# Kernel optimization log

Measured on AMD Instinct MI355X. Metric: run time of the kernel, lower is better.

Reference implementation:

```python
import jax, jax.numpy as jnp
import numpy as np

B = 2048
U_DIM = 128
N_USER = 500000
N_NEWS = 50000
N_WORD = 279215
TITLE_LEN = 10
W_EMB = 50
U_NB = 30   # user_neighbor
N_NB = 30   # news_neighbor
NCAPS = 8
NHID = 16
DIM = NCAPS * NHID          # 128
CNN_OUT = 128
ROUTIT = 4
CONV_CH, KH, KW = 8, 2, 20
PH, PW = 2, 1
FLAT = CONV_CH * ((TITLE_LEN - KH + 1) // PH) * (W_EMB - KW + 1)  # 8*4*31 = 992


def setup_inputs() -> dict:
    key = jax.random.key(0)
    ks = jax.random.split(key, 18)
    nrm = lambda k, s: jax.random.normal(k, s, jnp.float32) * 0.1
    return {
        "user_indices": jax.random.randint(ks[0], (B,), 0, N_USER),
        "news_indices": jax.random.randint(ks[1], (B,), 0, N_NEWS),
        "labels": (jax.random.uniform(ks[2], (B,)) > 0.5).astype(jnp.float32),
        # int neighbor / title tables (module buffers)
        "news_user": jax.random.randint(ks[3], (N_NEWS + 1, U_NB), 0, N_USER),
        "user_news": jax.random.randint(ks[4], (N_USER + 1, N_NB), 0, N_NEWS),
        "title": jax.random.randint(ks[5], (N_NEWS + 1, TITLE_LEN), 0, N_WORD),
        # float parameters
        "user_emb_matrix": nrm(ks[6], (N_USER + 1, U_DIM)),
        "word_emb_matrix": nrm(ks[7], (N_WORD + 1, W_EMB)),
        "conv_w": nrm(ks[8], (CONV_CH, 1, KH, KW)),
        "conv_b": jnp.zeros((CONV_CH,), jnp.float32),
        "dense_w": nrm(ks[9], (FLAT, CNN_OUT)),
        "dense_b": jnp.zeros((CNN_OUT,), jnp.float32),
        "user_weights": nrm(ks[10], (U_DIM, DIM)),
        "user_bias": nrm(ks[11], (DIM,)),
        "item_weights": nrm(ks[12], (CNN_OUT, DIM)),
        "item_bias": nrm(ks[13], (DIM,)),
        "last_w": nrm(ks[14], (DIM, DIM)),
        "last_b": jnp.zeros((DIM,), jnp.float32),
    }


def _convolution(news_ids, title, word_emb, conv_w, conv_b, dense_w, dense_b):
    """Title-CNN news encoder. news_ids: [B, K] int -> [B*K, CNN_OUT]."""
    bk = news_ids.shape[0] * news_ids.shape[1]
    words = title[news_ids.reshape(-1)]              # [BK, L] gather
    x = word_emb[words][:, None, :, :]               # [BK, 1, L, 50]
    y = jax.lax.conv_general_dilated(
        x, conv_w, (1, 1), 'VALID', dimension_numbers=('NCHW', 'OIHW', 'NCHW'))
    y = jax.nn.relu(y + conv_b[None, :, None, None])
    y = jax.lax.reduce_window(y, -jnp.inf, jax.lax.max,
                              (1, 1, PH, PW), (1, 1, PH, PW), 'VALID')
    return jax.nn.relu(y.reshape(bk, -1) @ dense_w + dense_b)


def _routing(x_self, z_nb):
    """Capsule neighbor routing. x_self: [B, DIM], z_nb: [B, K, DIM]."""
    l2n = lambda v: v / (jnp.linalg.norm(v, axis=-1, keepdims=True) + 1e-9)
    x = l2n(x_self.reshape(-1, NCAPS, NHID))
    z = l2n(z_nb.reshape(z_nb.shape[0], z_nb.shape[1], NCAPS, NHID))
    u = x
    for _ in range(ROUTIT):
        p = jax.nn.softmax(jnp.einsum('bkcd,bcd->bkc', z, u), axis=-1)  # over caps
        u = l2n(x + jnp.einsum('bkc,bkcd->bcd', p, z))
    return u.reshape(-1, DIM)


def reference(user_indices, news_indices, labels, news_user, user_news, title,
              user_emb_matrix, word_emb_matrix, conv_w, conv_b, dense_w, dense_b,
              user_weights, user_bias, item_weights, item_bias, last_w, last_b):
    # hop-0 (seed) vectors
    news_v0 = jax.nn.relu(
        _convolution(news_indices[:, None], title, word_emb_matrix,
                     conv_w, conv_b, dense_w, dense_b) @ item_weights + item_bias)  # [B, DIM]
    user_v0 = jax.nn.relu(user_emb_matrix[user_indices] @ user_weights + user_bias)  # [B, DIM]
    # hop-1 neighbor gathers
    news_nb = news_user[news_indices]   # [B, U_NB] user ids clicked this news
    user_nb = user_news[user_indices]   # [B, N_NB] news ids clicked by user
    news_v1 = jax.nn.relu(user_emb_matrix[news_nb] @ user_weights + user_bias)  # [B, U_NB, DIM]
    user_v1 = jax.nn.relu(
        _convolution(user_nb, title, word_emb_matrix, conv_w, conv_b,
                     dense_w, dense_b) @ item_weights + item_bias
    ).reshape(B, N_NB, DIM)
    # capsule routing aggregation
    news_emb = _routing(news_v0, news_v1)
    user_emb = _routing(user_v0, user_v1)
    # simple_dot_net scoring
    x_map = user_emb @ last_w + last_b
    y_map = news_emb @ last_w + last_b
    scores = jnp.sum(x_map * y_map, axis=-1)
    return jax.nn.sigmoid(scores)
```

## Files before the change

### kernel.cpp

```cpp
#include <hip/hip_runtime.h>
#include <hip/hip_bf16.h>
#include <math.h>

#define BSZ 2048
#define NNEWS 50000
#define U_NB 30
#define N_NB 30
#define TITLE_LEN 10
#define W_EMB 50
#define DIM 128
#define ROUTIT 4
#define FLAT2 1024

#define CONV_BLOCKS (NNEWS / 8)
#define PREP_ELEMS (DIM * FLAT2 + 2 * DIM * DIM)
#define PREP_BLOCKS (PREP_ELEMS / 256)
#define DENSE_BLOCKS ((NNEWS + 63) / 64)

typedef __attribute__((ext_vector_type(8))) short bf16x8;
typedef __attribute__((ext_vector_type(4))) float f32x4;

__device__ __forceinline__ ushort bfbits(float v) {
  __hip_bfloat16 h = __float2bfloat16(v);
  ushort u;
  __builtin_memcpy(&u, &h, 2);
  return u;
}

__device__ __forceinline__ bf16x8 bfrag(const ushort* row, int s) {
  const char* p = reinterpret_cast<const char*>(row) + ((s * 2) & ~15);
  const uint4 lo = *reinterpret_cast<const uint4*>(p);
  const uint4 hi = *reinterpret_cast<const uint4*>(p + 16);
  const uint d0 = lo.x, d1 = lo.y, d2 = lo.z, d3 = lo.w;
  const uint d4 = hi.x, d5 = hi.y, d6 = hi.z, d7 = hi.w;
  const bool q2 = (s & 4) != 0;
  const uint e0 = q2 ? d2 : d0, e1 = q2 ? d3 : d1, e2 = q2 ? d4 : d2;
  const uint e3 = q2 ? d5 : d3, e4 = q2 ? d6 : d4, e5 = q2 ? d7 : d5;
  const bool q1 = (s & 2) != 0;
  const uint f0 = q1 ? e1 : e0, f1 = q1 ? e2 : e1, f2 = q1 ? e3 : e2;
  const uint f3 = q1 ? e4 : e3, f4 = q1 ? e5 : e4;
  const bool r1 = (s & 1) != 0;
  uint g[4];
  g[0] = r1 ? ((f0 >> 16) | (f1 << 16)) : f0;
  g[1] = r1 ? ((f1 >> 16) | (f2 << 16)) : f1;
  g[2] = r1 ? ((f2 >> 16) | (f3 << 16)) : f2;
  g[3] = r1 ? ((f3 >> 16) | (f4 << 16)) : f3;
  bf16x8 r;
  __builtin_memcpy(&r, g, 16);
  return r;
}

__global__ __launch_bounds__(256, 4) void k_front(
    const int* __restrict__ title, const float* __restrict__ word_emb,
    const float* __restrict__ conv_w, const float* __restrict__ conv_b,
    const float* __restrict__ dw, const float* __restrict__ iw,
    const float* __restrict__ uw, __hip_bfloat16* __restrict__ flat,
    __hip_bfloat16* __restrict__ dwt, __hip_bfloat16* __restrict__ iwt,
    __hip_bfloat16* __restrict__ uwt) {
  const int tid = threadIdx.x;

  if (blockIdx.x >= CONV_BLOCKS) {
    const int idx = ((int)blockIdx.x - CONV_BLOCKS) * 256 + tid;
    if (idx < DIM * FLAT2) {
      const int col = idx & 127, k2 = idx >> 7;
      const int i = k2 & 3, X = k2 >> 2;
      const int c = X & 7, gkq = (X >> 3) & 3, jhq = (X >> 5) & 1, h = X >> 6;
      const int j = jhq * 16 + gkq * 4 + i;
      const float v = (j < 31) ? dw[(c * 124 + h * 31 + j) * 128 + col] : 0.f;
      dwt[col * FLAT2 + k2] = __float2bfloat16(v);
    } else if (idx < DIM * FLAT2 + DIM * DIM) {
      const int j = idx - DIM * FLAT2;
      const int o = j & 127, k = j >> 7;
      iwt[o * DIM + k] = __float2bfloat16(iw[j]);
    } else if (idx < PREP_ELEMS) {
      const int j = idx - DIM * FLAT2 - DIM * DIM;
      const int o = j & 127, k = j >> 7;
      uwt[o * DIM + k] = __float2bfloat16(uw[j]);
    }
    return;
  }

  __shared__ int s_words[80];
  __shared__ __align__(16) ushort s_x[80 * 64];

  const int wv = tid >> 6, lane = tid & 63;
  const int base = blockIdx.x * 8;
  const int c = lane & 15, gk = lane >> 4;

  bf16x8 b0, b1;
#pragma unroll
  for (int i = 0; i < 8; ++i) {
    const int k = gk * 8 + i;
    float v0 = 0.f, v1 = 0.f;
    if (c < 8 && k < 20) {
      v0 = conv_w[c * 40 + k];
      v1 = conv_w[c * 40 + 20 + k];
    }
    b0[i] = (short)bfbits(v0);
    b1[i] = (short)bfbits(v1);
  }
  const float cbias = (c < 8) ? conv_b[c] : 0.f;

  if (tid < 80) s_words[tid] = title[base * TITLE_LEN + tid];
  __syncthreads();

  {
    const float2* we2 = reinterpret_cast<const float2*>(word_emb);
#pragma unroll
    for (int i = 0; i < 3; ++i) {
      const int u = tid + i * 256;
      if (u < 640) {
        const int row = u >> 3, slot = u & 7;
        ushort o[8];
#pragma unroll
        for (int p = 0; p < 4; ++p) {
          const int c2 = slot * 4 + p;
          float2 v = make_float2(0.f, 0.f);
          if (c2 < 25) v = we2[(long long)s_words[row] * 25 + c2];
          o[2 * p] = bfbits(v.x);
          o[2 * p + 1] = bfbits(v.y);
        }
        *reinterpret_cast<uint4*>(&s_x[row * 64 + slot * 8]) =
            *reinterpret_cast<const uint4*>(o);
      }
    }
  }
  __syncthreads();

  ushort* fl = reinterpret_cast<ushort*>(flat);
#pragma unroll 1
  for (int tt = 0; tt < 2; ++tt) {
    const int t = wv * 2 + tt;
    const ushort* xb = &s_x[t * 640];
    ushort* gout = &fl[(size_t)(base + t) * FLAT2];
#pragma unroll
    for (int jh = 0; jh < 2; ++jh) {
      const int s = jh * 16 + (lane & 15) + gk * 8;
      bf16x8 fprev = bfrag(xb, s);
#pragma unroll
      for (int h = 0; h < 4; ++h) {
        const bf16x8 fmid = bfrag(xb + (2 * h + 1) * 64, s);
        const bf16x8 fnext = bfrag(xb + (2 * h + 2) * 64, s);
        f32x4 d0 = (f32x4){0.f, 0.f, 0.f, 0.f};
        f32x4 d1 = (f32x4){0.f, 0.f, 0.f, 0.f};
        d0 = __builtin_amdgcn_mfma_f32_16x16x32_bf16(fprev, b0, d0, 0, 0, 0);
        d0 = __builtin_amdgcn_mfma_f32_16x16x32_bf16(fmid, b1, d0, 0, 0, 0);
        d1 = __builtin_amdgcn_mfma_f32_16x16x32_bf16(fmid, b0, d1, 0, 0, 0);
        d1 = __builtin_amdgcn_mfma_f32_16x16x32_bf16(fnext, b1, d1, 0, 0, 0);
        if (c < 8) {
          ushort w[4];
#pragma unroll
          for (int i2 = 0; i2 < 4; ++i2)
            w[i2] = bfbits(fmaxf(fmaxf(d0[i2], d1[i2]) + cbias, 0.f));
          *reinterpret_cast<uint2*>(&gout[(h * 64 + jh * 32 + gk * 8 + c) * 4]) =
              *reinterpret_cast<const uint2*>(w);
        }
        fprev = fnext;
      }
    }
  }
}

__global__ __launch_bounds__(256, 2) void k_dense(
    const __hip_bfloat16* __restrict__ flat,
    const __hip_bfloat16* __restrict__ dwt, const float* __restrict__ dense_b,
    const __hip_bfloat16* __restrict__ iwt, const float* __restrict__ item_b,
    __hip_bfloat16* __restrict__ news_cnn) {
  __shared__ __align__(16) char lds[18432];
  ushort* A0 = (ushort*)lds;
  ushort* A1 = (ushort*)(lds + 9216);
  ushort* c1 = (ushort*)lds;

  const int tid = threadIdx.x;
  const int wv = tid >> 6, lane = tid & 63;
  const int fr = lane & 15, gk = lane >> 4;
  const int lrow0 = min((int)blockIdx.x * 64, NNEWS - 64);
  const ushort* fl = (const ushort*)flat;
  const ushort* dwp = (const ushort*)dwt;

  uint4 pA[2];
#define LD_A(KS)                                                              \
  {                                                                           \
    _Pragma("unroll") for (int q = 0; q < 2; ++q) {                           \
      const int uu = tid + q * 256;                                           \
      pA[q] = *reinterpret_cast<const uint4*>(                                \
          &fl[(size_t)(lrow0 + (uu >> 3)) * FLAT2 + (KS) * 64 + (uu & 7) * 8]); \
    }                                                                         \
  }
#define ST_A(BUF)                                                             \
  {                                                                           \
    _Pragma("unroll") for (int q = 0; q < 2; ++q) {                           \
      const int uu = tid + q * 256;                                           \
      *reinterpret_cast<uint4*>(&(BUF)[(uu >> 3) * 72 + (uu & 7) * 8]) = pA[q]; \
    }                                                                         \
  }
#define LD_B(DST, KS)                                                         \
  {                                                                           \
    _Pragma("unroll") for (int nn = 0; nn < 2; ++nn)                          \
        _Pragma("unroll") for (int qq = 0; qq < 2; ++qq) {                    \
      (DST)[nn * 2 + qq] = *reinterpret_cast<const bf16x8*>(                  \
          &dwp[(wv * 32 + nn * 16 + fr) * FLAT2 + (KS) * 64 + qq * 32 +       \
               gk * 8]);                                                      \
    }                                                                         \
  }

  LD_A(0);
  ST_A(A0);
  LD_A(1);
  bf16x8 bA[4];
  LD_B(bA, 0);
  __syncthreads();

  f32x4 acc[4][2];
#pragma unroll
  for (int m = 0; m < 4; ++m)
#pragma unroll
    for (int n2 = 0; n2 < 2; ++n2) acc[m][n2] = (f32x4){0.f, 0.f, 0.f, 0.f};

  for (int ks = 0; ks < 16; ++ks) {
    const ushort* cA = (ks & 1) ? A1 : A0;
    bf16x8 bN[4];
    if (ks < 15) {
      LD_B(bN, ks + 1);
    } else {
#pragma unroll
      for (int z = 0; z < 4; ++z) bN[z] = bA[z];
    }
    bf16x8 af[2][4];
#pragma unroll
    for (int kk = 0; kk < 2; ++kk)
#pragma unroll
      for (int m = 0; m < 4; ++m)
        af[kk][m] = *reinterpret_cast<const bf16x8*>(
            &cA[(m * 16 + fr) * 72 + kk * 32 + gk * 8]);
#pragma unroll
    for (int kk = 0; kk < 2; ++kk)
#pragma unroll
      for (int m = 0; m < 4; ++m)
#pragma unroll
        for (int n2 = 0; n2 < 2; ++n2)
          acc[m][n2] = __builtin_amdgcn_mfma_f32_16x16x32_bf16(
              af[kk][m], bA[n2 * 2 + kk], acc[m][n2], 0, 0, 0);
    if (ks < 15) {
      if (ks & 1) {
        ST_A(A0);
      } else {
        ST_A(A1);
      }
    }
    if (ks < 14) LD_A(ks + 2);
    __syncthreads();
#pragma unroll
    for (int z = 0; z < 4; ++z) bA[z] = bN[z];
  }
#undef LD_A
#undef ST_A
#undef LD_B

#pragma unroll
  for (int n2 = 0; n2 < 2; ++n2) {
    const int col = wv * 32 + n2 * 16 + fr;
    const float bb = dense_b[col];
#pragma unroll
    for (int m = 0; m < 4; ++m)
#pragma unroll
      for (int r = 0; r < 4; ++r)
        c1[(m * 16 + gk * 4 + r) * 136 + col] =
            bfbits(fmaxf(acc[m][n2][r] + bb, 0.f));
  }
  __syncthreads();

  const ushort* iwp = (const ushort*)iwt;
  f32x4 a2[4][2];
#pragma unroll
  for (int m = 0; m < 4; ++m)
#pragma unroll
    for (int n2 = 0; n2 < 2; ++n2) a2[m][n2] = (f32x4){0.f, 0.f, 0.f, 0.f};
#pragma unroll
  for (int kk = 0; kk < 4; ++kk) {
    bf16x8 af[4], bfr[2];
#pragma unroll
    for (int m = 0; m < 4; ++m)
      af[m] = *reinterpret_cast<const bf16x8*>(
          &c1[(m * 16 + fr) * 136 + kk * 32 + gk * 8]);
#pragma unroll
    for (int n2 = 0; n2 < 2; ++n2)
      bfr[n2] = *reinterpret_cast<const bf16x8*>(
          &iwp[(wv * 32 + n2 * 16 + fr) * DIM + kk * 32 + gk * 8]);
#pragma unroll
    for (int m = 0; m < 4; ++m)
#pragma unroll
      for (int n2 = 0; n2 < 2; ++n2)
        a2[m][n2] = __builtin_amdgcn_mfma_f32_16x16x32_bf16(
            af[m], bfr[n2], a2[m][n2], 0, 0, 0);
  }

#pragma unroll
  for (int n2 = 0; n2 < 2; ++n2) {
    const int col = wv * 32 + n2 * 16 + fr;
    const float bb = item_b[col];
#pragma unroll
    for (int m = 0; m < 4; ++m)
#pragma unroll
      for (int r = 0; r < 4; ++r) {
        const int row = m * 16 + gk * 4 + r;
        news_cnn[(size_t)(lrow0 + row) * DIM + col] =
            __float2bfloat16(fmaxf(a2[m][n2][r] + bb, 0.f));
      }
  }
}

__device__ __forceinline__ float gsum16(float v) {
  v += __shfl_xor(v, 1, 16);
  v += __shfl_xor(v, 2, 16);
  v += __shfl_xor(v, 4, 16);
  v += __shfl_xor(v, 8, 16);
  return v;
}

__global__ __launch_bounds__(512) void k_back(
    const __hip_bfloat16* __restrict__ news_cnn,
    const float* __restrict__ user_emb, const __hip_bfloat16* __restrict__ uwt,
    const float* __restrict__ user_b, const int* __restrict__ user_indices,
    const int* __restrict__ news_indices, const int* __restrict__ news_user,
    const int* __restrict__ user_news, const float* __restrict__ last_w,
    const float* __restrict__ last_b, float* __restrict__ out) {
  __shared__ int s_uid[32];
  __shared__ int s_nid[32];
  __shared__ __align__(16) __hip_bfloat16 s_e[32][136];
  __shared__ __align__(16) float zf2[2][30][132];
  __shared__ __align__(16) float xn2[2][128];
  __shared__ __align__(16) float uu2[2][128];
  __shared__ __align__(16) float pp2[2][30][8];
  __shared__ float s_r[2];

  const int b = blockIdx.x, tid = threadIdx.x;

  if (tid < 32) {
    int uid;
    if (tid == 0 || tid == 31)
      uid = user_indices[b];
    else
      uid = news_user[(long long)news_indices[b] * U_NB + (tid - 1)];
    s_uid[tid] = uid;
  }
  if (tid >= 64 && tid < 94)
    s_nid[tid - 64] = user_news[(long long)user_indices[b] * N_NB + (tid - 64)];
  __syncthreads();

  const int hs = tid >> 8;
  const int t = tid & 255;
  float(*zf)[132] = zf2[hs];
  float* xn = xn2[hs];
  float* uu = uu2[hs];
  float(*pp)[8] = pp2[hs];

  if (tid < 256) {
#pragma unroll
    for (int i = 0; i < 4; ++i) {
      const int u = tid + i * 256;
      const int row = u >> 5, d4 = u & 31;
      const float4 v = *reinterpret_cast<const float4*>(
          &user_emb[(long long)s_uid[row] * DIM + d4 * 4]);
      __hip_bfloat16* p = &s_e[row][d4 * 4];
      p[0] = __float2bfloat16(v.x);
      p[1] = __float2bfloat16(v.y);
      p[2] = __float2bfloat16(v.z);
      p[3] = __float2bfloat16(v.w);
    }
  } else {
    if (t < 240) {
      const int k = t >> 3, q = t & 7;
      const ushort* src =
          reinterpret_cast<const ushort*>(news_cnn + (long long)s_nid[k] * DIM);
      ushort h16[16];
      *reinterpret_cast<uint4*>(&h16[0]) =
          *reinterpret_cast<const uint4*>(&src[q * 16]);
      *reinterpret_cast<uint4*>(&h16[8]) =
          *reinterpret_cast<const uint4*>(&src[q * 16 + 8]);
      float f[16];
#pragma unroll
      for (int i = 0; i < 16; ++i) {
        const uint bits = ((uint)h16[i]) << 16;
        __builtin_memcpy(&f[i], &bits, 4);
      }
#pragma unroll
      for (int v4 = 0; v4 < 4; ++v4)
        *reinterpret_cast<f32x4*>(&zf2[1][k][q * 16 + v4 * 4]) =
            *reinterpret_cast<f32x4*>(&f[v4 * 4]);
    } else {
      const int j = t - 240;
      const ushort* src = reinterpret_cast<const ushort*>(
          news_cnn + (long long)news_indices[b] * DIM);
      ushort h8[8];
      *reinterpret_cast<uint4*>(h8) =
          *reinterpret_cast<const uint4*>(&src[j * 8]);
#pragma unroll
      for (int i = 0; i < 8; ++i) {
        const uint bits = ((uint)h8[i]) << 16;
        float fv;
        __builtin_memcpy(&fv, &bits, 4);
        xn2[0][j * 8 + i] = fv;
      }
    }
  }
  __syncthreads();

  float z16[16];
  const int kk = t >> 3, cc = t & 7;
  if (tid < 256) {
    const int wv = tid >> 6, lane = tid & 63;
    const int fr = lane & 15, gk = lane >> 4;
    const ushort* uwp = (const ushort*)uwt;
    f32x4 acc[2][2];
#pragma unroll
    for (int m = 0; m < 2; ++m)
#pragma unroll
      for (int n = 0; n < 2; ++n) acc[m][n] = (f32x4){0.f, 0.f, 0.f, 0.f};
#pragma unroll
    for (int ks = 0; ks < 4; ++ks) {
      bf16x8 af[2], bfr[2];
#pragma unroll
      for (int m = 0; m < 2; ++m)
        af[m] = *reinterpret_cast<const bf16x8*>(
            &s_e[m * 16 + fr][ks * 32 + gk * 8]);
#pragma unroll
      for (int n = 0; n < 2; ++n)
        bfr[n] = *reinterpret_cast<const bf16x8*>(
            &uwp[(wv * 32 + n * 16 + fr) * DIM + ks * 32 + gk * 8]);
#pragma unroll
      for (int m = 0; m < 2; ++m)
#pragma unroll
        for (int n = 0; n < 2; ++n)
          acc[m][n] = __builtin_amdgcn_mfma_f32_16x16x32_bf16(
              af[m], bfr[n], acc[m][n], 0, 0, 0);
    }
#pragma unroll
    for (int n = 0; n < 2; ++n) {
      const int col = wv * 32 + n * 16 + fr;
      const float bb = user_b[col];
#pragma unroll
      for (int m = 0; m < 2; ++m)
#pragma unroll
        for (int r = 0; r < 4; ++r) {
          const int row = m * 16 + gk * 4 + r;
          const float val = fmaxf(acc[m][n][r] + bb, 0.f);
          if (row == 0)
            xn2[1][col] = val;
          else if (row < 31)
            zf2[0][row - 1][col] = val;
        }
    }
  } else if (t < 240) {
    float ss = 0.f;
#pragma unroll
    for (int d = 0; d < 16; ++d) {
      z16[d] = zf2[1][kk][cc * 16 + d];
      ss += z16[d] * z16[d];
    }
    const float inv = 1.f / (sqrtf(ss) + 1e-9f);
#pragma unroll
    for (int d = 0; d < 16; ++d) {
      z16[d] *= inv;
      zf2[1][kk][cc * 16 + d] = z16[d];
    }
  }
  __syncthreads();

  if (hs == 0 && t < 240) {
    float ss = 0.f;
#pragma unroll
    for (int d = 0; d < 16; ++d) {
      z16[d] = zf2[0][kk][cc * 16 + d];
      ss += z16[d] * z16[d];
    }
    const float inv = 1.f / (sqrtf(ss) + 1e-9f);
#pragma unroll
    for (int d = 0; d < 16; ++d) {
      z16[d] *= inv;
      zf2[0][kk][cc * 16 + d] = z16[d];
    }
  }
  if (t < 128) {
    float xv = xn[t];
    xv = xv / (sqrtf(gsum16(xv * xv)) + 1e-9f);
    xn[t] = xv;
    uu[t] = xv;
  }
  __syncthreads();

  for (int it = 0; it < ROUTIT; ++it) {
    if (t < 240) {
      float dot = 0.f;
#pragma unroll
      for (int d = 0; d < 16; ++d) dot += z16[d] * uu[cc * 16 + d];
      float m8 = dot;
      m8 = fmaxf(m8, __shfl_xor(m8, 1, 8));
      m8 = fmaxf(m8, __shfl_xor(m8, 2, 8));
      m8 = fmaxf(m8, __shfl_xor(m8, 4, 8));
      float e = expf(dot - m8);
      float s8 = e;
      s8 += __shfl_xor(s8, 1, 8);
      s8 += __shfl_xor(s8, 2, 8);
      s8 += __shfl_xor(s8, 4, 8);
      pp[kk][cc] = e / s8;
    }
    __syncthreads();
    if (t < 128) {
      const int c2 = t >> 4;
      float agg = xn[t];
#pragma unroll
      for (int k = 0; k < 30; ++k) agg += pp[k][c2] * zf[k][t];
      uu[t] = agg / (sqrtf(gsum16(agg * agg)) + 1e-9f);
    }
    __syncthreads();
  }

  if (tid < 128) {
    float xm = last_b[tid], ym = xm;
    for (int k = 0; k < DIM; k += 4) {
#pragma unroll
      for (int i = 0; i < 4; ++i) {
        const float w = last_w[(k + i) * DIM + tid];
        xm += uu2[1][k + i] * w;
        ym += uu2[0][k + i] * w;
      }
    }
    float prod = xm * ym;
#pragma unroll
    for (int off = 1; off < 64; off <<= 1) prod += __shfl_xor(prod, off, 64);
    if ((tid & 63) == 0) s_r[tid >> 6] = prod;
  }
  __syncthreads();
  if (tid == 0) out[b] = 1.f / (1.f + expf(-(s_r[0] + s_r[1])));
}

extern "C" void kernel_launch(void* const* d_in, const int* in_sizes, int n_in,
                              void* d_out, int out_size, void* d_ws,
                              size_t ws_size, hipStream_t stream) {
  (void)in_sizes; (void)n_in; (void)out_size; (void)ws_size;
  const int* user_indices = (const int*)d_in[0];
  const int* news_indices = (const int*)d_in[1];
  const int* news_user = (const int*)d_in[3];
  const int* user_news = (const int*)d_in[4];
  const int* title = (const int*)d_in[5];
  const float* user_emb_matrix = (const float*)d_in[6];
  const float* word_emb_matrix = (const float*)d_in[7];
  const float* conv_w = (const float*)d_in[8];
  const float* conv_b = (const float*)d_in[9];
  const float* dense_w = (const float*)d_in[10];
  const float* dense_b = (const float*)d_in[11];
  const float* user_weights = (const float*)d_in[12];
  const float* user_bias = (const float*)d_in[13];
  const float* item_weights = (const float*)d_in[14];
  const float* item_bias = (const float*)d_in[15];
  const float* last_w = (const float*)d_in[16];
  const float* last_b = (const float*)d_in[17];

  char* ws = (char*)d_ws;
  __hip_bfloat16* flat = (__hip_bfloat16*)ws;
  ws += (size_t)NNEWS * FLAT2 * 2;
  __hip_bfloat16* news_cnn = (__hip_bfloat16*)ws;
  ws += (size_t)NNEWS * DIM * 2;
  __hip_bfloat16* dwt = (__hip_bfloat16*)ws;
  ws += (size_t)DIM * FLAT2 * 2;
  __hip_bfloat16* iwt = (__hip_bfloat16*)ws;
  ws += (size_t)DIM * DIM * 2;
  __hip_bfloat16* uwt = (__hip_bfloat16*)ws;
  float* out = (float*)d_out;

  k_front<<<CONV_BLOCKS + PREP_BLOCKS, 256, 0, stream>>>(
      title, word_emb_matrix, conv_w, conv_b, dense_w, item_weights,
      user_weights, flat, dwt, iwt, uwt);
  k_dense<<<DENSE_BLOCKS, 256, 0, stream>>>(flat, dwt, dense_b, iwt, item_bias,
                                            news_cnn);
  k_back<<<BSZ, 512, 0, stream>>>(news_cnn, user_emb_matrix, uwt, user_bias,
                                  user_indices, news_indices, news_user,
                                  user_news, last_w, last_b, out);
}
```

Measured before the change: 188.0 us.

## Fuse title convolution with dense layers to keep flat features in LDS

Merges the convolution kernel and the dense/item-projection kernel into one kernel that processes 16 news items per block. The flattened conv features stay in shared memory instead of being written to and reread from a 100MB global buffer. Weight preparation moves to its own small kernel. In exchange, each block now runs a 16-row M tile, so every block reloads the full dense weight matrix and there is less MFMA reuse per B fragment. The larger LDS footprint may also limit occupancy.

```diff
diff --git a/kernel.cpp b/kernel.cpp
--- a/kernel.cpp
+++ b/kernel.cpp
@@ -11,11 +11,11 @@
 #define DIM 128
 #define ROUTIT 4
 #define FLAT2 1024
-
-#define CONV_BLOCKS (NNEWS / 8)
+#define TPB 16
+#define SFLD 1032
+
 #define PREP_ELEMS (DIM * FLAT2 + 2 * DIM * DIM)
-#define PREP_BLOCKS (PREP_ELEMS / 256)
-#define DENSE_BLOCKS ((NNEWS + 63) / 64)
+#define NEWS_BLOCKS (NNEWS / TPB)
 
 typedef __attribute__((ext_vector_type(8))) short bf16x8;
 typedef __attribute__((ext_vector_type(4))) float f32x4;
@@ -50,42 +50,45 @@
   return r;
 }
 
-__global__ __launch_bounds__(256, 4) void k_front(
+__global__ __launch_bounds__(256) void k_prep(
+    const float* __restrict__ dw, const float* __restrict__ iw,
+    const float* __restrict__ uw, __hip_bfloat16* __restrict__ dwt,
+    __hip_bfloat16* __restrict__ iwt, __hip_bfloat16* __restrict__ uwt) {
+  const int idx = blockIdx.x * 256 + threadIdx.x;
+  if (idx < DIM * FLAT2) {
+    const int col = idx & 127, k2 = idx >> 7;
+    const int i = k2 & 3, X = k2 >> 2;
+    const int c = X & 7, gkq = (X >> 3) & 3, jhq = (X >> 5) & 1, h = X >> 6;
+    const int j = jhq * 16 + gkq * 4 + i;
+    const float v = (j < 31) ? dw[(c * 124 + h * 31 + j) * 128 + col] : 0.f;
+    dwt[col * FLAT2 + k2] = __float2bfloat16(v);
+  } else if (idx < DIM * FLAT2 + DIM * DIM) {
+    const int j = idx - DIM * FLAT2;
+    const int o = j & 127, k = j >> 7;
+    iwt[o * DIM + k] = __float2bfloat16(iw[j]);
+  } else if (idx < PREP_ELEMS) {
+    const int j = idx - DIM * FLAT2 - DIM * DIM;
+    const int o = j & 127, k = j >> 7;
+    uwt[o * DIM + k] = __float2bfloat16(uw[j]);
+  }
+}
+
+__global__ __launch_bounds__(256, 2) void k_news(
     const int* __restrict__ title, const float* __restrict__ word_emb,
     const float* __restrict__ conv_w, const float* __restrict__ conv_b,
-    const float* __restrict__ dw, const float* __restrict__ iw,
-    const float* __restrict__ uw, __hip_bfloat16* __restrict__ flat,
-    __hip_bfloat16* __restrict__ dwt, __hip_bfloat16* __restrict__ iwt,
-    __hip_bfloat16* __restrict__ uwt) {
+    const __hip_bfloat16* __restrict__ dwt, const float* __restrict__ dense_b,
+    const __hip_bfloat16* __restrict__ iwt, const float* __restrict__ item_b,
+    __hip_bfloat16* __restrict__ news_cnn) {
+  __shared__ int s_words[TPB * TITLE_LEN];
+  __shared__ __align__(16) ushort s_x[TPB * 640];
+  __shared__ __align__(16) ushort s_flat[TPB * SFLD];
+  ushort* c1 = s_x;
+
   const int tid = threadIdx.x;
-
-  if (blockIdx.x >= CONV_BLOCKS) {
-    const int idx = ((int)blockIdx.x - CONV_BLOCKS) * 256 + tid;
-    if (idx < DIM * FLAT2) {
-      const int col = idx & 127, k2 = idx >> 7;
-      const int i = k2 & 3, X = k2 >> 2;
-      const int c = X & 7, gkq = (X >> 3) & 3, jhq = (X >> 5) & 1, h = X >> 6;
-      const int j = jhq * 16 + gkq * 4 + i;
-      const float v = (j < 31) ? dw[(c * 124 + h * 31 + j) * 128 + col] : 0.f;
-      dwt[col * FLAT2 + k2] = __float2bfloat16(v);
-    } else if (idx < DIM * FLAT2 + DIM * DIM) {
-      const int j = idx - DIM * FLAT2;
-      const int o = j & 127, k = j >> 7;
-      iwt[o * DIM + k] = __float2bfloat16(iw[j]);
-    } else if (idx < PREP_ELEMS) {
-      const int j = idx - DIM * FLAT2 - DIM * DIM;
-      const int o = j & 127, k = j >> 7;
-      uwt[o * DIM + k] = __float2bfloat16(uw[j]);
-    }
-    return;
-  }
-
-  __shared__ int s_words[80];
-  __shared__ __align__(16) ushort s_x[80 * 64];
-
   const int wv = tid >> 6, lane = tid & 63;
-  const int base = blockIdx.x * 8;
+  const int base = blockIdx.x * TPB;
   const int c = lane & 15, gk = lane >> 4;
+  const int fr = lane & 15;
 
   bf16x8 b0, b1;
 #pragma unroll
@@ -101,99 +104,69 @@
   }
   const float cbias = (c < 8) ? conv_b[c] : 0.f;
 
-  if (tid < 80) s_words[tid] = title[base * TITLE_LEN + tid];
+  if (tid < TPB * TITLE_LEN) s_words[tid] = title[base * TITLE_LEN + tid];
   __syncthreads();
 
   {
     const float2* we2 = reinterpret_cast<const float2*>(word_emb);
 #pragma unroll
-    for (int i = 0; i < 3; ++i) {
+    for (int i = 0; i < 5; ++i) {
       const int u = tid + i * 256;
-      if (u < 640) {
-        const int row = u >> 3, slot = u & 7;
-        ushort o[8];
-#pragma unroll
-        for (int p = 0; p < 4; ++p) {
-          const int c2 = slot * 4 + p;
-          float2 v = make_float2(0.f, 0.f);
-          if (c2 < 25) v = we2[(long long)s_words[row] * 25 + c2];
-          o[2 * p] = bfbits(v.x);
-          o[2 * p + 1] = bfbits(v.y);
+      const int row = u >> 3, slot = u & 7;
+      ushort o[8];
+#pragma unroll
+      for (int p = 0; p < 4; ++p) {
+        const int c2 = slot * 4 + p;
+        float2 v = make_float2(0.f, 0.f);
+        if (c2 < 25) v = we2[(long long)s_words[row] * 25 + c2];
+        o[2 * p] = bfbits(v.x);
+        o[2 * p + 1] = bfbits(v.y);
+      }
+      *reinterpret_cast<uint4*>(&s_x[row * 64 + slot * 8]) =
+          *reinterpret_cast<const uint4*>(o);
+    }
+  }
+  __syncthreads();
+
+#pragma unroll 1
+  for (int p = 0; p < 2; ++p) {
+#pragma unroll 1
+    for (int tt = 0; tt < 2; ++tt) {
+      const int t = p * 8 + wv * 2 + tt;
+      const ushort* xb = &s_x[t * 640];
+      ushort* fout = &s_flat[t * SFLD];
+#pragma unroll
+      for (int jh = 0; jh < 2; ++jh) {
+        const int s = jh * 16 + fr + gk * 8;
+        bf16x8 fprev = bfrag(xb, s);
+#pragma unroll
+        for (int h = 0; h < 4; ++h) {
+          const bf16x8 fmid = bfrag(xb + (2 * h + 1) * 64, s);
+          const bf16x8 fnext = bfrag(xb + (2 * h + 2) * 64, s);
+          f32x4 d0 = (f32x4){0.f, 0.f, 0.f, 0.f};
+          f32x4 d1 = (f32x4){0.f, 0.f, 0.f, 0.f};
+          d0 = __builtin_amdgcn_mfma_f32_16x16x32_bf16(fprev, b0, d0, 0, 0, 0);
+          d0 = __builtin_amdgcn_mfma_f32_16x16x32_bf16(fmid, b1, d0, 0, 0, 0);
+          d1 = __builtin_amdgcn_mfma_f32_16x16x32_bf16(fmid, b0, d1, 0, 0, 0);
+          d1 = __builtin_amdgcn_mfma_f32_16x16x32_bf16(fnext, b1, d1, 0, 0, 0);
+          if (c < 8) {
+            ushort w[4];
+#pragma unroll
+            for (int i2 = 0; i2 < 4; ++i2)
+              w[i2] = bfbits(fmaxf(fmaxf(d0[i2], d1[i2]) + cbias, 0.f));
+            *reinterpret_cast<uint2*>(
+                &fout[(h * 64 + jh * 32 + gk * 8 + c) * 4]) =
+                *reinterpret_cast<const uint2*>(w);
+          }
+          fprev = fnext;
         }
-        *reinterpret_cast<uint4*>(&s_x[row * 64 + slot * 8]) =
-            *reinterpret_cast<const uint4*>(o);
       }
     }
   }
   __syncthreads();
 
-  ushort* fl = reinterpret_cast<ushort*>(flat);
-#pragma unroll 1
-  for (int tt = 0; tt < 2; ++tt) {
-    const int t = wv * 2 + tt;
-    const ushort* xb = &s_x[t * 640];
-    ushort* gout = &fl[(size_t)(base + t) * FLAT2];
-#pragma unroll
-    for (int jh = 0; jh < 2; ++jh) {
-      const int s = jh * 16 + (lane & 15) + gk * 8;
-      bf16x8 fprev = bfrag(xb, s);
-#pragma unroll
-      for (int h = 0; h < 4; ++h) {
-        const bf16x8 fmid = bfrag(xb + (2 * h + 1) * 64, s);
-        const bf16x8 fnext = bfrag(xb + (2 * h + 2) * 64, s);
-        f32x4 d0 = (f32x4){0.f, 0.f, 0.f, 0.f};
-        f32x4 d1 = (f32x4){0.f, 0.f, 0.f, 0.f};
-        d0 = __builtin_amdgcn_mfma_f32_16x16x32_bf16(fprev, b0, d0, 0, 0, 0);
-        d0 = __builtin_amdgcn_mfma_f32_16x16x32_bf16(fmid, b1, d0, 0, 0, 0);
-        d1 = __builtin_amdgcn_mfma_f32_16x16x32_bf16(fmid, b0, d1, 0, 0, 0);
-        d1 = __builtin_amdgcn_mfma_f32_16x16x32_bf16(fnext, b1, d1, 0, 0, 0);
-        if (c < 8) {
-          ushort w[4];
-#pragma unroll
-          for (int i2 = 0; i2 < 4; ++i2)
-            w[i2] = bfbits(fmaxf(fmaxf(d0[i2], d1[i2]) + cbias, 0.f));
-          *reinterpret_cast<uint2*>(&gout[(h * 64 + jh * 32 + gk * 8 + c) * 4]) =
-              *reinterpret_cast<const uint2*>(w);
-        }
-        fprev = fnext;
-      }
-    }
-  }
-}
-
-__global__ __launch_bounds__(256, 2) void k_dense(
-    const __hip_bfloat16* __restrict__ flat,
-    const __hip_bfloat16* __restrict__ dwt, const float* __restrict__ dense_b,
-    const __hip_bfloat16* __restrict__ iwt, const float* __restrict__ item_b,
-    __hip_bfloat16* __restrict__ news_cnn) {
-  __shared__ __align__(16) char lds[18432];
-  ushort* A0 = (ushort*)lds;
-  ushort* A1 = (ushort*)(lds + 9216);
-  ushort* c1 = (ushort*)lds;
-
-  const int tid = threadIdx.x;
-  const int wv = tid >> 6, lane = tid & 63;
-  const int fr = lane & 15, gk = lane >> 4;
-  const int lrow0 = min((int)blockIdx.x * 64, NNEWS - 64);
-  const ushort* fl = (const ushort*)flat;
   const ushort* dwp = (const ushort*)dwt;
-
-  uint4 pA[2];
-#define LD_A(KS)                                                              \
-  {                                                                           \
-    _Pragma("unroll") for (int q = 0; q < 2; ++q) {                           \
-      const int uu = tid + q * 256;                                           \
-      pA[q] = *reinterpret_cast<const uint4*>(                                \
-          &fl[(size_t)(lrow0 + (uu >> 3)) * FLAT2 + (KS) * 64 + (uu & 7) * 8]); \
-    }                                                                         \
-  }
-#define ST_A(BUF)                                                             \
-  {                                                                           \
-    _Pragma("unroll") for (int q = 0; q < 2; ++q) {                           \
-      const int uu = tid + q * 256;                                           \
-      *reinterpret_cast<uint4*>(&(BUF)[(uu >> 3) * 72 + (uu & 7) * 8]) = pA[q]; \
-    }                                                                         \
-  }
+  bf16x8 bA[4], bN[4];
 #define LD_B(DST, KS)                                                         \
   {                                                                           \
     _Pragma("unroll") for (int nn = 0; nn < 2; ++nn)                          \
@@ -203,110 +176,69 @@
                gk * 8]);                                                      \
     }                                                                         \
   }
-
-  LD_A(0);
-  ST_A(A0);
-  LD_A(1);
-  bf16x8 bA[4];
   LD_B(bA, 0);
-  __syncthreads();
-
-  f32x4 acc[4][2];
-#pragma unroll
-  for (int m = 0; m < 4; ++m)
-#pragma unroll
-    for (int n2 = 0; n2 < 2; ++n2) acc[m][n2] = (f32x4){0.f, 0.f, 0.f, 0.f};
+  f32x4 acc[2];
+  acc[0] = (f32x4){0.f, 0.f, 0.f, 0.f};
+  acc[1] = (f32x4){0.f, 0.f, 0.f, 0.f};
 
   for (int ks = 0; ks < 16; ++ks) {
-    const ushort* cA = (ks & 1) ? A1 : A0;
-    bf16x8 bN[4];
     if (ks < 15) {
       LD_B(bN, ks + 1);
-    } else {
-#pragma unroll
-      for (int z = 0; z < 4; ++z) bN[z] = bA[z];
-    }
-    bf16x8 af[2][4];
+    }
+    bf16x8 af[2];
 #pragma unroll
     for (int kk = 0; kk < 2; ++kk)
-#pragma unroll
-      for (int m = 0; m < 4; ++m)
-        af[kk][m] = *reinterpret_cast<const bf16x8*>(
-            &cA[(m * 16 + fr) * 72 + kk * 32 + gk * 8]);
+      af[kk] = *reinterpret_cast<const bf16x8*>(
+          &s_flat[fr * SFLD + ks * 64 + kk * 32 + gk * 8]);
 #pragma unroll
     for (int kk = 0; kk < 2; ++kk)
 #pragma unroll
-      for (int m = 0; m < 4; ++m)
-#pragma unroll
-        for (int n2 = 0; n2 < 2; ++n2)
-          acc[m][n2] = __builtin_amdgcn_mfma_f32_16x16x32_bf16(
-              af[kk][m], bA[n2 * 2 + kk], acc[m][n2], 0, 0, 0);
+      for (int n = 0; n < 2; ++n)
+        acc[n] = __builtin_amdgcn_mfma_f32_16x16x32_bf16(af[kk], bA[n * 2 + kk],
+                                                         acc[n], 0, 0, 0);
     if (ks < 15) {
-      if (ks & 1) {
-        ST_A(A0);
-      } else {
-        ST_A(A1);
-      }
-    }
-    if (ks < 14) LD_A(ks + 2);
-    __syncthreads();
-#pragma unroll
-    for (int z = 0; z < 4; ++z) bA[z] = bN[z];
-  }
-#undef LD_A
-#undef ST_A
+#pragma unroll
+      for (int z = 0; z < 4; ++z) bA[z] = bN[z];
+    }
+  }
 #undef LD_B
-
-#pragma unroll
-  for (int n2 = 0; n2 < 2; ++n2) {
-    const int col = wv * 32 + n2 * 16 + fr;
+  __syncthreads();
+
+#pragma unroll
+  for (int n = 0; n < 2; ++n) {
+    const int col = wv * 32 + n * 16 + fr;
     const float bb = dense_b[col];
 #pragma unroll
-    for (int m = 0; m < 4; ++m)
-#pragma unroll
-      for (int r = 0; r < 4; ++r)
-        c1[(m * 16 + gk * 4 + r) * 136 + col] =
-            bfbits(fmaxf(acc[m][n2][r] + bb, 0.f));
+    for (int r = 0; r < 4; ++r)
+      c1[(gk * 4 + r) * 136 + col] = bfbits(fmaxf(acc[n][r] + bb, 0.f));
   }
   __syncthreads();
 
   const ushort* iwp = (const ushort*)iwt;
-  f32x4 a2[4][2];
-#pragma unroll
-  for (int m = 0; m < 4; ++m)
-#pragma unroll
-    for (int n2 = 0; n2 < 2; ++n2) a2[m][n2] = (f32x4){0.f, 0.f, 0.f, 0.f};
+  f32x4 a2[2];
+  a2[0] = (f32x4){0.f, 0.f, 0.f, 0.f};
+  a2[1] = (f32x4){0.f, 0.f, 0.f, 0.f};
 #pragma unroll
   for (int kk = 0; kk < 4; ++kk) {
-    bf16x8 af[4], bfr[2];
-#pragma unroll
-    for (int m = 0; m < 4; ++m)
-      af[m] = *reinterpret_cast<const bf16x8*>(
-          &c1[(m * 16 + fr) * 136 + kk * 32 + gk * 8]);
-#pragma unroll
-    for (int n2 = 0; n2 < 2; ++n2)
-      bfr[n2] = *reinterpret_cast<const bf16x8*>(
-          &iwp[(wv * 32 + n2 * 16 + fr) * DIM + kk * 32 + gk * 8]);
-#pragma unroll
-    for (int m = 0; m < 4; ++m)
-#pragma unroll
-      for (int n2 = 0; n2 < 2; ++n2)
-        a2[m][n2] = __builtin_amdgcn_mfma_f32_16x16x32_bf16(
-            af[m], bfr[n2], a2[m][n2], 0, 0, 0);
-  }
-
-#pragma unroll
-  for (int n2 = 0; n2 < 2; ++n2) {
-    const int col = wv * 32 + n2 * 16 + fr;
+    const bf16x8 af = *reinterpret_cast<const bf16x8*>(
+        &c1[fr * 136 + kk * 32 + gk * 8]);
+#pragma unroll
+    for (int n = 0; n < 2; ++n) {
+      const bf16x8 bfr = *reinterpret_cast<const bf16x8*>(
+          &iwp[(wv * 32 + n * 16 + fr) * DIM + kk * 32 + gk * 8]);
+      a2[n] = __builtin_amdgcn_mfma_f32_16x16x32_bf16(af, bfr, a2[n], 0, 0, 0);
+    }
+  }
+#pragma unroll
+  for (int n = 0; n < 2; ++n) {
+    const int col = wv * 32 + n * 16 + fr;
     const float bb = item_b[col];
 #pragma unroll
-    for (int m = 0; m < 4; ++m)
-#pragma unroll
-      for (int r = 0; r < 4; ++r) {
-        const int row = m * 16 + gk * 4 + r;
-        news_cnn[(size_t)(lrow0 + row) * DIM + col] =
-            __float2bfloat16(fmaxf(a2[m][n2][r] + bb, 0.f));
-      }
+    for (int r = 0; r < 4; ++r) {
+      const int row = gk * 4 + r;
+      news_cnn[(size_t)(base + row) * DIM + col] =
+          __float2bfloat16(fmaxf(a2[n][r] + bb, 0.f));
+    }
   }
 }
 
@@ -558,8 +490,6 @@
   const float* last_b = (const float*)d_in[17];
 
   char* ws = (char*)d_ws;
-  __hip_bfloat16* flat = (__hip_bfloat16*)ws;
-  ws += (size_t)NNEWS * FLAT2 * 2;
   __hip_bfloat16* news_cnn = (__hip_bfloat16*)ws;
   ws += (size_t)NNEWS * DIM * 2;
   __hip_bfloat16* dwt = (__hip_bfloat16*)ws;
@@ -569,11 +499,11 @@
   __hip_bfloat16* uwt = (__hip_bfloat16*)ws;
   float* out = (float*)d_out;
 
-  k_front<<<CONV_BLOCKS + PREP_BLOCKS, 256, 0, stream>>>(
-      title, word_emb_matrix, conv_w, conv_b, dense_w, item_weights,
-      user_weights, flat, dwt, iwt, uwt);
-  k_dense<<<DENSE_BLOCKS, 256, 0, stream>>>(flat, dwt, dense_b, iwt, item_bias,
-                                            news_cnn);
+  k_prep<<<(PREP_ELEMS + 255) / 256, 256, 0, stream>>>(
+      dense_w, item_weights, user_weights, dwt, iwt, uwt);
+  k_news<<<NEWS_BLOCKS, 256, 0, stream>>>(
+      title, word_emb_matrix, conv_w, conv_b, dwt, dense_b, iwt, item_bias,
+      news_cnn);
   k_back<<<BSZ, 512, 0, stream>>>(news_cnn, user_emb_matrix, uwt, user_bias,
                                   user_indices, news_indices, news_user,
                                   user_news, last_w, last_b, out);
```

New measurement: 245.8 us. +30.7%, slower.
